# Kernel optimization log

Hardware: AMD Instinct MI355X
Metric: run time of the kernel (lower is better)

## Reference

```python
import jax, jax.numpy as jnp
import numpy as np

B, T, C, H = 128, 256, 384, 6
HS = C // H  # 64
EPS = 1e-5


def _ln(x, g, b):
    mu = jnp.mean(x, axis=-1, keepdims=True)
    var = jnp.mean(jnp.square(x - mu), axis=-1, keepdims=True)
    return (x - mu) * jax.lax.rsqrt(var + EPS) * g + b


def setup_inputs() -> dict:
    key = jax.random.key(0)
    ks = jax.random.split(key, 12)
    s = 0.02
    return {
        "x": jax.random.normal(ks[0], (B, T, C), jnp.float32),
        "wq": jax.random.normal(ks[1], (H, C, HS), jnp.float32) * s,
        "wk": jax.random.normal(ks[2], (H, C, HS), jnp.float32) * s,
        "wv": jax.random.normal(ks[3], (H, C, HS), jnp.float32) * s,
        "w_proj": jax.random.normal(ks[4], (C, C), jnp.float32) * s,
        "b_proj": jax.random.normal(ks[5], (C,), jnp.float32) * s,
        "w1": jax.random.normal(ks[6], (C, 4 * C), jnp.float32) * s,
        "b1": jax.random.normal(ks[7], (4 * C,), jnp.float32) * s,
        "w2": jax.random.normal(ks[8], (4 * C, C), jnp.float32) * s,
        "b2": jax.random.normal(ks[9], (C,), jnp.float32) * s,
        "ln1_g": 1.0 + jax.random.normal(ks[10], (C,), jnp.float32) * s,
        "ln1_b": jnp.zeros((C,), jnp.float32),
        "ln2_g": 1.0 + jax.random.normal(ks[11], (C,), jnp.float32) * s,
        "ln2_b": jnp.zeros((C,), jnp.float32),
    }


def reference(x, wq, wk, wv, w_proj, b_proj, w1, b1, w2, b2, ln1_g, ln1_b, ln2_g, ln2_b):
    # --- attention sublayer (dropout = identity, eval mode) ---
    h = _ln(x, ln1_g, ln1_b)                              # (B,T,C)
    q = jnp.einsum("btc,hcd->bhtd", h, wq)               # (B,H,T,HS)
    k = jnp.einsum("btc,hcd->bhtd", h, wk)
    v = jnp.einsum("btc,hcd->bhtd", h, wv)
    # NOTE: original scales by n_embed**-0.5 (C), not head_size**-0.5
    wei = jnp.einsum("bhtd,bhsd->bhts", q, k) * (C ** -0.5)  # (B,H,T,T)
    tril = jnp.tril(jnp.ones((T, T), bool))
    wei = jnp.where(tril, wei, -jnp.inf)
    # NOTE: original applies softmax over torch dim=1 of (B,T,T) = query axis
    wei = jax.nn.softmax(wei, axis=2)
    attn = jnp.einsum("bhts,bhsd->bhtd", wei, v)          # (B,H,T,HS)
    attn = attn.transpose(0, 2, 1, 3).reshape(B, T, C)    # head-concat order
    x = x + attn @ w_proj + b_proj
    # --- MLP sublayer ---
    h2 = _ln(x, ln2_g, ln2_b)
    x = x + jax.nn.relu(h2 @ w1 + b1) @ w2 + b2
    return x
```

## Files before the change

### kernel.cpp

```cpp
#include <hip/hip_runtime.h>

#define BB 128
#define TT 256
#define CCH 384
#define NHH 6
#define HSZ 64
#define BTT (BB*TT)
#define QKVLD 1152

typedef unsigned short u16;
typedef unsigned int   u32;
typedef __attribute__((ext_vector_type(8))) short  short8;
typedef __attribute__((ext_vector_type(4))) float  floatx4;

__device__ __forceinline__ u16 f2bf(float f) {
  union { float f; u32 i; } v; v.f = f; u32 x = v.i;
  return (u16)((x + 0x7fffu + ((x >> 16) & 1u)) >> 16);
}
__device__ __forceinline__ float bf2f(u16 w) {
  union { u32 i; float f; } v; v.i = ((u32)w) << 16; return v.f;
}

__device__ __forceinline__ void gll16(const u16* g, u16* l) {
  __builtin_amdgcn_global_load_lds((const __attribute__((address_space(1))) void*)g,
                                   (__attribute__((address_space(3))) void*)l, 16, 0, 0);
}

template <int INBF>
__global__ __launch_bounds__(256) void ln_kernel(const void* __restrict__ xv,
                                                 const float* __restrict__ g,
                                                 const float* __restrict__ b,
                                                 u16* __restrict__ out) {
  int row = blockIdx.x * 4 + (threadIdx.x >> 6);
  int lane = threadIdx.x & 63;
  float vals[6];
  float sum = 0.f;
  if (INBF) {
    const u16* xr = (const u16*)xv + (size_t)row * CCH;
#pragma unroll
    for (int i = 0; i < 6; ++i) { vals[i] = bf2f(xr[lane + (i << 6)]); sum += vals[i]; }
  } else {
    const float* xr = (const float*)xv + (size_t)row * CCH;
#pragma unroll
    for (int i = 0; i < 6; ++i) { vals[i] = xr[lane + (i << 6)]; sum += vals[i]; }
  }
#pragma unroll
  for (int off = 32; off; off >>= 1) sum += __shfl_xor(sum, off);
  float mean = sum * (1.f / 384.f);
  float vs = 0.f;
#pragma unroll
  for (int i = 0; i < 6; ++i) { float d = vals[i] - mean; vs += d * d; }
#pragma unroll
  for (int off = 32; off; off >>= 1) vs += __shfl_xor(vs, off);
  float rinv = rsqrtf(vs * (1.f / 384.f) + 1e-5f);
  u16* orow = out + (size_t)row * CCH;
#pragma unroll
  for (int i = 0; i < 6; ++i) {
    int c = lane + (i << 6);
    orow[c] = f2bf((vals[i] - mean) * rinv * g[c] + b[c]);
  }
}

__global__ void repack_all(const float* __restrict__ wq, const float* __restrict__ wk,
                           const float* __restrict__ wv, const float* __restrict__ wproj,
                           const float* __restrict__ w1, const float* __restrict__ w2,
                           u16* __restrict__ wqkv_t, u16* __restrict__ wp_t,
                           u16* __restrict__ w1_t, u16* __restrict__ w2_t) {
  int idx = blockIdx.x * 256 + threadIdx.x;
  const int S1 = 442368;
  const int S2 = S1 + 147456;
  const int S3 = S2 + 589824;
  const int S4 = S3 + 589824;
  if (idx < S1) {
    int i = idx, e = i & 7, l = (i >> 3) & 63, r = i >> 9;
    int kt = r % 12, nb = r / 12;
    int n = nb * 16 + (l & 15), k = kt * 32 + (l >> 4) * 8 + e;
    int sel = n / 384, nn = n % 384;
    size_t src = ((size_t)(nn >> 6) * 384 + k) * 64 + (nn & 63);
    float v = (sel == 0) ? wq[src] : (sel == 1) ? wk[src] : wv[src];
    wqkv_t[i] = f2bf(v);
  } else if (idx < S2) {
    int i = idx - S1, e = i & 7, l = (i >> 3) & 63, r = i >> 9;
    int kt = r % 12, nb = r / 12;
    int n = nb * 16 + (l & 15), k = kt * 32 + (l >> 4) * 8 + e;
    wp_t[i] = f2bf(wproj[(size_t)k * 384 + n]);
  } else if (idx < S3) {
    int i = idx - S2, e = i & 7, l = (i >> 3) & 63, r = i >> 9;
    int kt = r % 12, nb = r / 12;
    int n = nb * 16 + (l & 15), k = kt * 32 + (l >> 4) * 8 + e;
    w1_t[i] = f2bf(w1[(size_t)k * 1536 + n]);
  } else if (idx < S4) {
    int i = idx - S3, e = i & 7, l = (i >> 3) & 63, r = i >> 9;
    int kt = r % 48, nb = r / 48;
    int n = nb * 16 + (l & 15), k = kt * 32 + (l >> 4) * 8 + e;
    w2_t[i] = f2bf(w2[(size_t)k * 384 + n]);
  }
}

template <int BIAS, int RES, int RELU, int OUTBF, int RESBF>
__global__ __launch_bounds__(256, 3) void gemm_mfma(const u16* __restrict__ A,
                                                    const u16* __restrict__ Bp,
                                                    const float* __restrict__ bias,
                                                    const void* __restrict__ resv,
                                                    void* __restrict__ outv,
                                                    int M, int N, int K) {
  __shared__ __align__(16) u16 As[2][128 * 32];
  const int tid = threadIdx.x;
  const int lane = tid & 63;
  const int w = tid >> 6;
  const int wr = w >> 1, wc = w & 1;

  const int gx = gridDim.x;
  const int nwg = gx * gridDim.y;
  const int bid = blockIdx.y * gx + blockIdx.x;
  const int lin = (bid & 7) * (nwg >> 3) + (bid >> 3);
  const int m0 = (lin / gx) * 128, n0 = (lin % gx) * 128;

  const int lm = lane & 15, qd = lane >> 4;
  const int KT = K >> 5;

  floatx4 acc[4][4];
  floatx4 zero4 = {0.f, 0.f, 0.f, 0.f};
#pragma unroll
  for (int i = 0; i < 4; ++i)
#pragma unroll
    for (int j = 0; j < 4; ++j) acc[i][j] = zero4;

  const u16* srcA[2];
#pragma unroll
  for (int c = 0; c < 2; ++c) {
    int row = 32 * w + 16 * c + (lane >> 2);
    int ch = (lane & 3) ^ ((row >> 1) & 3);
    srcA[c] = A + (size_t)(m0 + row) * K + ch * 8;
  }
  const int dA = (32 * w) * 32;

  const u16* bsrc[4];
#pragma unroll
  for (int j = 0; j < 4; ++j)
    bsrc[j] = Bp + ((size_t)((n0 >> 4) + 4 * wc + j) * KT) * 512 + lane * 8;

#pragma unroll
  for (int c = 0; c < 2; ++c) gll16(srcA[c], &As[0][dA + 512 * c]);
  short8 bcur[4], bnxt[4];
#pragma unroll
  for (int j = 0; j < 4; ++j) bcur[j] = *(const short8*)(bsrc[j]);

  for (int k0 = 0; k0 < K; k0 += 64) {
    __syncthreads();
    {
      int kn = k0 + 32;
      int kto = (kn >> 5) << 9;
#pragma unroll
      for (int j = 0; j < 4; ++j) bnxt[j] = *(const short8*)(bsrc[j] + kto);
#pragma unroll
      for (int c = 0; c < 2; ++c) gll16(srcA[c] + kn, &As[1][dA + 512 * c]);
      short8 af[4];
#pragma unroll
      for (int i = 0; i < 4; ++i) {
        int rm = 64 * wr + 16 * i + lm;
        af[i] = *(const short8*)&As[0][rm * 32 + (qd ^ ((rm >> 1) & 3)) * 8];
      }
#pragma unroll
      for (int i = 0; i < 4; ++i)
#pragma unroll
        for (int j = 0; j < 4; ++j)
          acc[i][j] = __builtin_amdgcn_mfma_f32_16x16x32_bf16(af[i], bcur[j], acc[i][j], 0, 0, 0);
    }
    __syncthreads();
    {
      int kn = k0 + 64;
      if (kn < K) {
        int kto = (kn >> 5) << 9;
#pragma unroll
        for (int j = 0; j < 4; ++j) bcur[j] = *(const short8*)(bsrc[j] + kto);
#pragma unroll
        for (int c = 0; c < 2; ++c) gll16(srcA[c] + kn, &As[0][dA + 512 * c]);
      }
      short8 af[4];
#pragma unroll
      for (int i = 0; i < 4; ++i) {
        int rm = 64 * wr + 16 * i + lm;
        af[i] = *(const short8*)&As[1][rm * 32 + (qd ^ ((rm >> 1) & 3)) * 8];
      }
#pragma unroll
      for (int i = 0; i < 4; ++i)
#pragma unroll
        for (int j = 0; j < 4; ++j)
          acc[i][j] = __builtin_amdgcn_mfma_f32_16x16x32_bf16(af[i], bnxt[j], acc[i][j], 0, 0, 0);
    }
  }

#pragma unroll
  for (int i = 0; i < 4; ++i) {
    int row0 = m0 + 64 * wr + 16 * i + qd * 4;
#pragma unroll
    for (int j = 0; j < 4; ++j) {
      int col = n0 + 64 * wc + 16 * j + lm;
      float bb = 0.f;
      if (BIAS) bb = bias[col];
#pragma unroll
      for (int r = 0; r < 4; ++r) {
        size_t idx = (size_t)(row0 + r) * N + col;
        float val = acc[i][j][r] + bb;
        if (RES) val += RESBF ? bf2f(((const u16*)resv)[idx]) : ((const float*)resv)[idx];
        if (RELU) val = fmaxf(val, 0.f);
        if (OUTBF) ((u16*)outv)[idx] = f2bf(val);
        else       ((float*)outv)[idx] = val;
      }
    }
  }
}

#define ASCALE 0.051031036307982884f

__global__ __launch_bounds__(1024) void attn_mfma(const u16* __restrict__ qkv,
                                                  u16* __restrict__ out) {
  __shared__ __align__(16) char lds_raw[36864 + 20480 + 2048];
  u16*   Ks       = (u16*)lds_raw;
  u16*   VT       = (u16*)lds_raw;
  float* partials = (float*)(lds_raw + 36864);
  u16*   stage    = (u16*)(lds_raw + 36864);
  float* gmax     = (float*)(lds_raw + 57344);
  float* linv     = (float*)(lds_raw + 58368);

  const int tid = threadIdx.x;
  const int lane = tid & 63;
  const int w = tid >> 6;
  const int lm = lane & 15, qd = lane >> 4;
  const int b = blockIdx.x / NHH, h = blockIdx.x % NHH;
  const size_t rowbase = (size_t)b * TT;
  const u16* qp = qkv + rowbase * QKVLD + h * HSZ;
  const u16* kp = qp + 384;
  const u16* vp = qp + 768;

  {
    int s = tid >> 2, c4 = tid & 3;
    const u16* src = kp + (size_t)s * QKVLD;
    *(uint4*)&Ks[s * 72 + c4 * 8]       = *(const uint4*)(src + c4 * 8);
    *(uint4*)&Ks[s * 72 + (c4 + 4) * 8] = *(const uint4*)(src + (c4 + 4) * 8);
  }
  short8 qf0, qf1;
  {
    const u16* qrow = qp + (size_t)(16 * w + lm) * QKVLD + qd * 8;
    qf0 = *(const short8*)(qrow);
    qf1 = *(const short8*)(qrow + 32);
  }
  __syncthreads();

  floatx4 acc[16];
  floatx4 zero4 = {0.f, 0.f, 0.f, 0.f};
#pragma unroll
  for (int tc = 0; tc < 16; ++tc) acc[tc] = zero4;

#pragma unroll
  for (int tc = 0; tc < 16; ++tc) {
    if (tc <= w) {
      int sr = 16 * tc + lm;
      short8 kf0 = *(const short8*)&Ks[sr * 72 + qd * 8];
      short8 kf1 = *(const short8*)&Ks[sr * 72 + 32 + qd * 8];
      acc[tc] = __builtin_amdgcn_mfma_f32_16x16x32_bf16(qf0, kf0, acc[tc], 0, 0, 0);
      acc[tc] = __builtin_amdgcn_mfma_f32_16x16x32_bf16(qf1, kf1, acc[tc], 0, 0, 0);
    }
  }

  const int rb = 16 * w + qd * 4;
  float pmax[16];
#pragma unroll
  for (int tc = 0; tc < 16; ++tc) {
    float m = -1e30f;
    if (tc <= w) {
      int sc = 16 * tc + lm;
#pragma unroll
      for (int r = 0; r < 4; ++r) {
        float vv = acc[tc][r] * ASCALE;
        vv = (rb + r >= sc) ? vv : -1e30f;
        acc[tc][r] = vv;
        m = fmaxf(m, vv);
      }
    }
    m = fmaxf(m, __shfl_xor(m, 16));
    m = fmaxf(m, __shfl_xor(m, 32));
    pmax[tc] = m;
  }
  if (lane < 16) {
#pragma unroll
    for (int tc = 0; tc < 16; ++tc) partials[w * 256 + tc * 16 + lane] = pmax[tc];
  }
  __syncthreads();
  if (tid < 256) {
    float m = partials[tid];
#pragma unroll
    for (int i = 1; i < 16; ++i) m = fmaxf(m, partials[i * 256 + tid]);
    gmax[tid] = m;
  }
  __syncthreads();

  float psum[16];
#pragma unroll
  for (int tc = 0; tc < 16; ++tc) {
    float s = 0.f;
    if (tc <= w) {
      float gm = gmax[tc * 16 + lm];
#pragma unroll
      for (int r = 0; r < 4; ++r) {
        float e = (acc[tc][r] > -1e29f) ? __expf(acc[tc][r] - gm) : 0.f;
        acc[tc][r] = e;
        s += e;
      }
    }
    s += __shfl_xor(s, 16);
    s += __shfl_xor(s, 32);
    psum[tc] = s;
  }
  if (lane < 16) {
#pragma unroll
    for (int tc = 0; tc < 16; ++tc) partials[w * 256 + tc * 16 + lane] = psum[tc];
  }
  __syncthreads();
  if (tid < 256) {
    float s = partials[tid];
#pragma unroll
    for (int i = 1; i < 16; ++i) s += partials[i * 256 + tid];
    linv[tid] = 1.f / s;
  }
  __syncthreads();

  {
    int s = tid >> 2, dg = (tid & 3) * 16;
    const u16* vrow = vp + (size_t)s * QKVLD + dg;
    u16 tmp[16];
    *(uint4*)&tmp[0] = *(const uint4*)(vrow);
    *(uint4*)&tmp[8] = *(const uint4*)(vrow + 8);
#pragma unroll
    for (int j = 0; j < 16; ++j) VT[(dg + j) * 264 + s] = tmp[j];
  }
  __syncthreads();

  u16* mst = stage + w * 640;
  floatx4 oacc[4];
#pragma unroll
  for (int nt = 0; nt < 4; ++nt) oacc[nt] = zero4;

#pragma unroll
  for (int c = 0; c < 8; ++c) {
    if (2 * c <= w) {
#pragma unroll
      for (int tt = 0; tt < 2; ++tt) {
        int tc = 2 * c + tt;
        float li = (tc <= w) ? linv[tc * 16 + lm] : 0.f;
#pragma unroll
        for (int r = 0; r < 4; ++r) {
          float pv = (tc <= w) ? acc[tc][r] * li : 0.f;
          mst[(qd * 4 + r) * 40 + tt * 16 + lm] = f2bf(pv);
        }
      }
      asm volatile("s_waitcnt lgkmcnt(0)" ::: "memory");
      short8 pf = *(const short8*)&mst[lm * 40 + qd * 8];
#pragma unroll
      for (int nt = 0; nt < 4; ++nt) {
        short8 vf = *(const short8*)&VT[(nt * 16 + lm) * 264 + c * 32 + qd * 8];
        oacc[nt] = __builtin_amdgcn_mfma_f32_16x16x32_bf16(pf, vf, oacc[nt], 0, 0, 0);
      }
      asm volatile("" ::: "memory");
    }
  }

  u16* ob = out + rowbase * CCH + h * HSZ;
#pragma unroll
  for (int nt = 0; nt < 4; ++nt) {
#pragma unroll
    for (int r = 0; r < 4; ++r) {
      int t = 16 * w + qd * 4 + r;
      ob[(size_t)t * CCH + nt * 16 + lm] = f2bf(oacc[nt][r]);
    }
  }
}

extern "C" void kernel_launch(void* const* d_in, const int* in_sizes, int n_in,
                              void* d_out, int out_size, void* d_ws, size_t ws_size,
                              hipStream_t stream) {
  const float* x     = (const float*)d_in[0];
  const float* wq    = (const float*)d_in[1];
  const float* wk    = (const float*)d_in[2];
  const float* wv    = (const float*)d_in[3];
  const float* wproj = (const float*)d_in[4];
  const float* bproj = (const float*)d_in[5];
  const float* w1    = (const float*)d_in[6];
  const float* b1    = (const float*)d_in[7];
  const float* w2    = (const float*)d_in[8];
  const float* b2    = (const float*)d_in[9];
  const float* ln1g  = (const float*)d_in[10];
  const float* ln1b  = (const float*)d_in[11];
  const float* ln2g  = (const float*)d_in[12];
  const float* ln2b  = (const float*)d_in[13];
  float* out = (float*)d_out;
  (void)in_sizes; (void)n_in; (void)out_size; (void)ws_size;

  char* ws = (char*)d_ws;
  size_t off = 0;
  auto alloc = [&](size_t bytes) -> void* {
    void* p = ws + off;
    off += (bytes + 255) & ~(size_t)255;
    return p;
  };

  u16* wqkv_t = (u16*)alloc((size_t)QKVLD * CCH * 2);
  u16* wp_t   = (u16*)alloc((size_t)CCH * CCH * 2);
  u16* w1_t   = (u16*)alloc((size_t)4 * CCH * CCH * 2);
  u16* w2_t   = (u16*)alloc((size_t)CCH * 4 * CCH * 2);
  u16*   h_b  = (u16*)alloc((size_t)BTT * CCH * 2);
  u16*   x2   = (u16*)alloc((size_t)BTT * CCH * 2);
  u16*   qkv_b = (u16*)alloc((size_t)BTT * 4 * CCH * 2);
  u16*   u_b   = qkv_b;

  repack_all<<<6912, 256, 0, stream>>>(wq, wk, wv, wproj, w1, w2,
                                       wqkv_t, wp_t, w1_t, w2_t);

  ln_kernel<0><<<BTT / 4, 256, 0, stream>>>(x, ln1g, ln1b, h_b);

  gemm_mfma<0, 0, 0, 1, 0><<<dim3(9, 256), 256, 0, stream>>>(h_b, wqkv_t, nullptr, nullptr,
                                                             qkv_b, BTT, QKVLD, CCH);
  attn_mfma<<<BB * NHH, 1024, 0, stream>>>(qkv_b, h_b);

  gemm_mfma<1, 1, 0, 1, 0><<<dim3(3, 256), 256, 0, stream>>>(h_b, wp_t, bproj, x, x2,
                                                             BTT, CCH, CCH);
  ln_kernel<1><<<BTT / 4, 256, 0, stream>>>(x2, ln2g, ln2b, h_b);

  gemm_mfma<1, 0, 1, 1, 0><<<dim3(12, 256), 256, 0, stream>>>(h_b, w1_t, b1, nullptr, u_b,
                                                              BTT, 4 * CCH, CCH);
  gemm_mfma<1, 1, 0, 0, 1><<<dim3(3, 256), 256, 0, stream>>>(u_b, w2_t, b2, x2, out,
                                                             BTT, CCH, 4 * CCH);
}
```

Measured before the change: 339.6 us.

## Add K-resident GEMM kernel for K=384 projections with full A tile in LDS

```diff
diff --git a/kernel.cpp b/kernel.cpp
--- a/kernel.cpp
+++ b/kernel.cpp
@@ -98,6 +98,117 @@
 }
 
 template <int BIAS, int RES, int RELU, int OUTBF, int RESBF>
+__global__ __launch_bounds__(256, 3) void gemm_kres(const u16* __restrict__ A,
+                                                    const u16* __restrict__ Bp,
+                                                    const float* __restrict__ bias,
+                                                    const void* __restrict__ resv,
+                                                    void* __restrict__ outv,
+                                                    int M, int N) {
+  __shared__ __align__(16) u16 Ah[64 * 384];
+  const int tid = threadIdx.x;
+  const int lane = tid & 63;
+  const int w = tid >> 6;
+  const int wr = w >> 1, wc = w & 1;
+
+  const int gx = gridDim.x;
+  const int nwg = gx * gridDim.y;
+  const int bid = blockIdx.y * gx + blockIdx.x;
+  const int lin = (bid & 7) * (nwg >> 3) + (bid >> 3);
+  const int m0 = (lin / gx) * 64, n0 = (lin % gx) * 128;
+
+  const int lm = lane & 15, qd = lane >> 4;
+
+#pragma unroll
+  for (int rnd = 0; rnd < 12; ++rnd) {
+    int wbase = rnd * 2048 + w * 512;
+    int off = wbase + lane * 8;
+    int row = off / 384;
+    int slot = (off - row * 384) >> 3;
+    const u16* src = A + (size_t)(m0 + row) * 384 + ((slot ^ (row & 7)) << 3);
+    gll16(src, &Ah[wbase]);
+  }
+
+  const u16* bsrc[4];
+#pragma unroll
+  for (int j = 0; j < 4; ++j)
+    bsrc[j] = Bp + ((size_t)((n0 >> 4) + 4 * wc + j) * 12) * 512 + lane * 8;
+
+  floatx4 acc[2][4];
+  floatx4 zero4 = {0.f, 0.f, 0.f, 0.f};
+#pragma unroll
+  for (int i = 0; i < 2; ++i)
+#pragma unroll
+    for (int j = 0; j < 4; ++j) acc[i][j] = zero4;
+
+  short8 bA[4], bB[4];
+#pragma unroll
+  for (int j = 0; j < 4; ++j) bA[j] = *(const short8*)(bsrc[j]);
+
+  asm volatile("s_waitcnt vmcnt(0)" ::: "memory");
+  __syncthreads();
+
+#pragma unroll
+  for (int k2 = 0; k2 < 6; ++k2) {
+    {
+      const int kt = 2 * k2;
+#pragma unroll
+      for (int j = 0; j < 4; ++j) bB[j] = *(const short8*)(bsrc[j] + (kt + 1) * 512);
+      short8 af[2];
+#pragma unroll
+      for (int i = 0; i < 2; ++i) {
+        int row = 32 * wr + 16 * i + lm;
+        int s = (kt * 4 + qd) ^ (row & 7);
+        af[i] = *(const short8*)&Ah[row * 384 + s * 8];
+      }
+#pragma unroll
+      for (int i = 0; i < 2; ++i)
+#pragma unroll
+        for (int j = 0; j < 4; ++j)
+          acc[i][j] = __builtin_amdgcn_mfma_f32_16x16x32_bf16(af[i], bA[j], acc[i][j], 0, 0, 0);
+    }
+    {
+      const int kt = 2 * k2 + 1;
+      if (kt < 11) {
+#pragma unroll
+        for (int j = 0; j < 4; ++j) bA[j] = *(const short8*)(bsrc[j] + (kt + 1) * 512);
+      }
+      short8 af[2];
+#pragma unroll
+      for (int i = 0; i < 2; ++i) {
+        int row = 32 * wr + 16 * i + lm;
+        int s = (kt * 4 + qd) ^ (row & 7);
+        af[i] = *(const short8*)&Ah[row * 384 + s * 8];
+      }
+#pragma unroll
+      for (int i = 0; i < 2; ++i)
+#pragma unroll
+        for (int j = 0; j < 4; ++j)
+          acc[i][j] = __builtin_amdgcn_mfma_f32_16x16x32_bf16(af[i], bB[j], acc[i][j], 0, 0, 0);
+    }
+  }
+
+#pragma unroll
+  for (int i = 0; i < 2; ++i) {
+    int row0 = m0 + 32 * wr + 16 * i + qd * 4;
+#pragma unroll
+    for (int j = 0; j < 4; ++j) {
+      int col = n0 + 64 * wc + 16 * j + lm;
+      float bb = 0.f;
+      if (BIAS) bb = bias[col];
+#pragma unroll
+      for (int r = 0; r < 4; ++r) {
+        size_t idx = (size_t)(row0 + r) * N + col;
+        float val = acc[i][j][r] + bb;
+        if (RES) val += RESBF ? bf2f(((const u16*)resv)[idx]) : ((const float*)resv)[idx];
+        if (RELU) val = fmaxf(val, 0.f);
+        if (OUTBF) ((u16*)outv)[idx] = f2bf(val);
+        else       ((float*)outv)[idx] = val;
+      }
+    }
+  }
+}
+
+template <int BIAS, int RES, int RELU, int OUTBF, int RESBF>
 __global__ __launch_bounds__(256, 3) void gemm_mfma(const u16* __restrict__ A,
                                                     const u16* __restrict__ Bp,
                                                     const float* __restrict__ bias,
@@ -419,16 +530,16 @@
 
   ln_kernel<0><<<BTT / 4, 256, 0, stream>>>(x, ln1g, ln1b, h_b);
 
-  gemm_mfma<0, 0, 0, 1, 0><<<dim3(9, 256), 256, 0, stream>>>(h_b, wqkv_t, nullptr, nullptr,
-                                                             qkv_b, BTT, QKVLD, CCH);
+  gemm_kres<0, 0, 0, 1, 0><<<dim3(9, 512), 256, 0, stream>>>(h_b, wqkv_t, nullptr, nullptr,
+                                                             qkv_b, BTT, QKVLD);
   attn_mfma<<<BB * NHH, 1024, 0, stream>>>(qkv_b, h_b);
 
-  gemm_mfma<1, 1, 0, 1, 0><<<dim3(3, 256), 256, 0, stream>>>(h_b, wp_t, bproj, x, x2,
-                                                             BTT, CCH, CCH);
+  gemm_kres<1, 1, 0, 1, 0><<<dim3(3, 512), 256, 0, stream>>>(h_b, wp_t, bproj, x, x2,
+                                                             BTT, CCH);
   ln_kernel<1><<<BTT / 4, 256, 0, stream>>>(x2, ln2g, ln2b, h_b);
 
-  gemm_mfma<1, 0, 1, 1, 0><<<dim3(12, 256), 256, 0, stream>>>(h_b, w1_t, b1, nullptr, u_b,
-                                                              BTT, 4 * CCH, CCH);
+  gemm_kres<1, 0, 1, 1, 0><<<dim3(12, 512), 256, 0, stream>>>(h_b, w1_t, b1, nullptr, u_b,
+                                                              BTT, 4 * CCH);
   gemm_mfma<1, 1, 0, 0, 1><<<dim3(3, 256), 256, 0, stream>>>(u_b, w2_t, b2, x2, out,
                                                              BTT, CCH, 4 * CCH);
 }
```

Result: slower. 353.6 us (+4.1%).
